# Optimization experiments

Measured on AMD Instinct MI355X. Metric: run time of the kernel, lower is better.

## Reference

```python
import jax, jax.numpy as jnp
import numpy as np

B_SZ, L_MAX, T_LEN, D = 512, 48, 128, 300   # sentences, graph slots, tokens, glove_dim
N_A, N_C = 2048, 2048                        # aspect rows, clause rows
H, TOP_K = 4, 96                             # attention heads, top-k over flattened LxL


def setup_inputs() -> dict:
    key = jax.random.key(0)
    ks = jax.random.split(key, 8)
    input_embed = jax.random.normal(ks[0], (B_SZ, T_LEN, D), jnp.float32)
    clause_output = jax.random.normal(ks[1], (N_C, D), jnp.float32)
    batch_aa_mask = (jax.random.uniform(ks[2], (N_A, T_LEN)) < 0.5).astype(jnp.float32)
    aa_graph_length = jax.random.randint(ks[3], (B_SZ,), 1, L_MAX + 1, dtype=jnp.int32)
    # collision-free scatter destinations; maxima hit B_SZ-1 and L_MAX-1 exactly
    map_AA = jnp.arange(N_A, dtype=jnp.int32) % B_SZ
    map_AA_idx = (4 + jnp.arange(N_A, dtype=jnp.int32) // B_SZ).at[-1].set(L_MAX - 1)
    map_AS = jnp.arange(N_C, dtype=jnp.int32) % B_SZ
    map_AS_idx = jnp.arange(N_C, dtype=jnp.int32) // B_SZ
    sc = 1.0 / np.sqrt(D).astype(np.float32)
    Wq = jax.random.normal(ks[4], (D, D), jnp.float32) * sc
    Wk = jax.random.normal(ks[5], (D, D), jnp.float32) * sc
    Wg = jax.random.normal(ks[6], (D, D), jnp.float32) * sc
    bq = jnp.zeros((D,), jnp.float32)
    bk = jnp.zeros((D,), jnp.float32)
    bg = jnp.zeros((D,), jnp.float32)
    return {"input_embed": input_embed, "clause_output": clause_output,
            "batch_aa_mask": batch_aa_mask, "aa_graph_length": aa_graph_length,
            "map_AA": map_AA, "map_AA_idx": map_AA_idx,
            "map_AS": map_AS, "map_AS_idx": map_AS_idx,
            "Wq": Wq, "bq": bq, "Wk": Wk, "bk": bk, "Wg": Wg, "bg": bg}


def reference(input_embed, clause_output, batch_aa_mask, aa_graph_length,
              map_AA, map_AA_idx, map_AS, map_AS_idx, Wq, bq, Wk, bk, Wg, bg):
    B, L = B_SZ, L_MAX
    dk = D // H
    # gather sentence tokens per aspect, masked sum over tokens -> [Na, D]
    aa_embed = jnp.einsum('ntd,nt->nd', input_embed[map_AA], batch_aa_mask)
    # scatter aspect and clause features into the [B, L, D] graph tensor
    inner = jnp.zeros((B, L, D), input_embed.dtype)
    inner = inner.at[map_AA, map_AA_idx].set(aa_embed)
    inner = inner.at[map_AS, map_AS_idx].set(clause_output)
    mask_indi = (jnp.arange(L)[None, :] < aa_graph_length[:, None]).astype(inner.dtype)  # [B,L]
    # attention-based adjacency (scores only, softmax over keys)
    q = (inner @ Wq.T + bq).reshape(B, L, H, dk).transpose(0, 2, 1, 3)
    k = (inner @ Wk.T + bk).reshape(B, L, H, dk).transpose(0, 2, 1, 3)
    scores = jnp.einsum('bhid,bhjd->bhij', q, k) / jnp.sqrt(jnp.asarray(dk, inner.dtype))
    scores = jnp.where(mask_indi[:, None, None, :] == 0, -1e9, scores)
    attn = jax.nn.softmax(scores, axis=-1)                      # [B,H,L,L]
    # average heads, replace diagonal with self-loops, zero padded rows
    adj = attn.mean(axis=1)
    eye = jnp.eye(L, dtype=adj.dtype)
    adj = adj * (1.0 - eye) + eye
    adj = adj * mask_indi[:, :, None]
    # top-k sparsify over flattened adjacency, symmetrize, diag=1, reweight
    flat = adj.reshape(B, L * L)
    kth = jax.lax.top_k(flat, TOP_K)[0][:, -1]                  # [B]
    sel = (flat >= kth[:, None]).astype(adj.dtype).reshape(B, L, L)
    sel = sel + sel.transpose(0, 2, 1)
    sel = sel * (1.0 - eye) + eye
    adj = sel * adj
    # one GCN layer: relu(W(A x) / (rowsum(A)+1))
    denom = adj.sum(axis=-1, keepdims=True) + 1.0
    gcn = jax.nn.relu((jnp.einsum('bij,bjd->bid', adj, inner) @ Wg.T + bg) / denom)
    # gather back to clause rows; keep clause_output where graph has <=1 node
    aa_out = gcn[map_AS, map_AS_idx]                            # [Nc, D]
    need = (aa_graph_length[map_AS] > 1)[:, None]
    return jnp.where(need, aa_out, clause_output)
```

## Files before the change

### kernel.cpp

```cpp
#include <hip/hip_runtime.h>
#include <math.h>

#define B_SZ 512
#define LG 48
#define T_LEN 128
#define DIM 300
#define NA 2048
#define NC 2048
#define NH 4
#define DK 75
#define KTOP 96
#define ACAP 16
#define TM 64
#define TN 64
#define WSS 156
#define QKS 608
#define GTM 32
#define GTN 64
#define GKC 60
#define FCAP2 9
#define SSTR 612

__global__ __launch_bounds__(256) void build_kernel(
    const int* __restrict__ mapAA, const int* __restrict__ mapAAi,
    int* __restrict__ slot_src, int* __restrict__ acnt, int* __restrict__ alist) {
  int n = blockIdx.x * 256 + threadIdx.x;
  if (n >= NA) return;
  int b = mapAA[n];
  atomicMax(&slot_src[b * LG + mapAAi[n]], n);
  int pos = atomicAdd(&acnt[b], 1);
  if (pos < ACAP) alist[b * ACAP + pos] = n;
}

__global__ __launch_bounds__(256) void aspect_kernel(
    const float* __restrict__ embed, const float* __restrict__ mask,
    const int* __restrict__ acnt, const int* __restrict__ alist,
    float* __restrict__ X) {
  int b = blockIdx.x;
  int na = acnt[b]; if (na > ACAP) na = ACAP;
  if (na == 0) return;
  __shared__ float mLds[ACAP][T_LEN];
  __shared__ float4 eLds[32][DK];
  int tid = threadIdx.x;
  for (int i = tid; i < na * T_LEN; i += 256) {
    int k = i / T_LEN, t = i - k * T_LEN;
    mLds[k][t] = mask[(size_t)alist[b * ACAP + k] * T_LEN + t];
  }
  int nw = na * DK;
  int i0 = tid, i1 = tid + 256;
  int k0 = i0 / DK, d0 = i0 - k0 * DK;
  int k1 = i1 / DK, d1 = i1 - k1 * DK;
  float4 a0 = {0, 0, 0, 0}, a1 = {0, 0, 0, 0};
  const float4* e4 = (const float4*)(embed + (size_t)b * T_LEN * DIM);
  for (int t0 = 0; t0 < T_LEN; t0 += 32) {
    __syncthreads();
    for (int i = tid; i < 32 * DK; i += 256) {
      int t = i / DK, d = i - t * DK;
      eLds[t][d] = e4[(size_t)(t0 + t) * DK + d];
    }
    __syncthreads();
#pragma unroll
    for (int t = 0; t < 32; ++t) {
      if (i0 < nw) {
        float m = mLds[k0][t0 + t]; float4 ev = eLds[t][d0];
        a0.x += m * ev.x; a0.y += m * ev.y; a0.z += m * ev.z; a0.w += m * ev.w;
      }
      if (i1 < nw) {
        float m = mLds[k1][t0 + t]; float4 ev = eLds[t][d1];
        a1.x += m * ev.x; a1.y += m * ev.y; a1.z += m * ev.z; a1.w += m * ev.w;
      }
    }
  }
  if (i0 < nw) ((float4*)(X + (size_t)alist[b * ACAP + k0] * DIM))[d0] = a0;
  if (i1 < nw) ((float4*)(X + (size_t)alist[b * ACAP + k1] * DIM))[d1] = a1;
}

__global__ __launch_bounds__(128) void clause_kernel(
    const float* __restrict__ clause, const int* __restrict__ mapAS,
    const int* __restrict__ mapASi, float* __restrict__ X,
    int* __restrict__ slot_src) {
  int n = blockIdx.x, t = threadIdx.x;
  const float4* src = (const float4*)(clause + (size_t)n * DIM);
  float4* dst = (float4*)(X + (size_t)(NA + n) * DIM);
  if (t < DIM / 4) dst[t] = src[t];
  if (t == 96) atomicMax(&slot_src[mapAS[n] * LG + mapASi[n]], NA + n);
}

__global__ __launch_bounds__(256) void qk_kernel(
    const float* __restrict__ X, const float* __restrict__ Wq,
    const float* __restrict__ Wk, float* __restrict__ QKP) {
  __shared__ __align__(16) float ws[TN][WSS];
  int z = blockIdx.z;
  int kbase = z ? 152 : 0;
  int ng = z ? 37 : 38;
  int m0 = blockIdx.x * TM, n0 = blockIdx.y * TN;
  int tid = threadIdx.x;
  int ty = tid >> 4;
  int tx = tid & 15;
  float acc[4][4];
#pragma unroll
  for (int a = 0; a < 4; ++a)
#pragma unroll
    for (int c = 0; c < 4; ++c) acc[a][c] = 0.f;

  for (int i = tid; i < TN * ng; i += 256) {
    int c = i / ng, g = i - c * ng;
    int col = n0 + c;
    float4 v = {0.f, 0.f, 0.f, 0.f};
    if (col < 2 * DIM) {
      const float* w = (col < DIM) ? (Wq + (size_t)col * DIM)
                                   : (Wk + (size_t)(col - DIM) * DIM);
      v = *(const float4*)&w[kbase + g * 4];
    }
    *(float4*)&ws[c][g * 4] = v;
  }
  __syncthreads();

  const float* xrow[4];
#pragma unroll
  for (int a = 0; a < 4; ++a)
    xrow[a] = X + (size_t)(m0 + ty * 4 + a) * DIM + kbase;

#pragma unroll 2
  for (int kg = 0; kg < ng; ++kg) {
    float4 xv[4], wv[4];
#pragma unroll
    for (int a = 0; a < 4; ++a) xv[a] = *(const float4*)&xrow[a][kg * 4];
#pragma unroll
    for (int c = 0; c < 4; ++c) wv[c] = *(const float4*)&ws[tx + 16 * c][kg * 4];
#pragma unroll
    for (int a = 0; a < 4; ++a)
#pragma unroll
      for (int c = 0; c < 4; ++c)
        acc[a][c] += wv[c].x * xv[a].x + wv[c].y * xv[a].y +
                     wv[c].z * xv[a].z + wv[c].w * xv[a].w;
  }

  float* out = QKP + (size_t)z * (NA + NC) * QKS;
#pragma unroll
  for (int cc = 0; cc < 4; ++cc) {
    int col = n0 + tx + 16 * cc;
    if (col < 2 * DIM) {
      int off;
      if (col < DIM) off = col + col / DK;
      else { int c2 = col - DIM; off = 304 + c2 + c2 / DK; }
#pragma unroll
      for (int a = 0; a < 4; ++a)
        out[(size_t)(m0 + ty * 4 + a) * QKS + off] = acc[a][cc];
    }
  }
}

__global__ __launch_bounds__(512) void attn2_kernel(
    const float* __restrict__ QKP, const float* __restrict__ X,
    const float* __restrict__ bq, const float* __restrict__ bk,
    const int* __restrict__ slot_src, const int* __restrict__ aa_len,
    float* __restrict__ xout, float* __restrict__ dng, int* __restrict__ mdg) {
  int b = blockIdx.x, tid = threadIdx.x;
  __shared__ __align__(16) float staged[FCAP2][SSTR];
  __shared__ float buf4[NH][LG][LG + 1];
  __shared__ float coef[4][LG], denomc[4];
  __shared__ int srcs[LG], nlist[LG], flist[LG], qrow[LG];
  __shared__ float kthL;
  __shared__ int sh_nneed, sh_nf;

  int length = aa_len[b];
  if (length > LG) length = LG;
  if (tid < LG) srcs[tid] = slot_src[b * LG + tid];
  __syncthreads();

  if (tid < 64) {
    bool isneed = (tid < LG) && (srcs[tid] >= NA);
    unsigned long long nm = __ballot(isneed);
    if (isneed) nlist[__popcll(nm & ((1ull << tid) - 1ull))] = tid;
    bool isf = (tid < LG) && (srcs[tid] >= 0);
    unsigned long long fm = __ballot(isf);
    int nf = __popcll(fm);
    if (nf > FCAP2 - 1) nf = FCAP2 - 1;
    if (isf) {
      int c = __popcll(fm & ((1ull << tid) - 1ull));
      if (c < FCAP2 - 1) flist[c] = tid;
    }
    if (tid < LG) {
      int c = __popcll(fm & ((1ull << tid) - 1ull));
      qrow[tid] = (isf && c < FCAP2 - 1) ? c : nf;
    }
    if (tid == 0) { sh_nneed = __popcll(nm); sh_nf = nf; }
  }
  __syncthreads();
  int nneed = sh_nneed, nf = sh_nf;

  if (length <= 1) {
    if (tid < nneed) mdg[srcs[nlist[tid]] - NA] = 0;
    return;
  }

  for (int j = tid; j < 608; j += 512) {
    int half = (j >= 304) ? 1 : 0;
    int jj = j - half * 304;
    int h = jj / 76, d = jj - h * 76;
    float v = 0.f;
    if (d < DK) v = half ? bk[h * DK + d] : bq[h * DK + d];
    staged[nf][j] = v;
  }
  __syncthreads();
  {
    const float* P0 = QKP;
    const float* P1 = QKP + (size_t)(NA + NC) * QKS;
    for (int i = tid; i < nf * 152; i += 512) {
      int m = i / 152, g = i - m * 152;
      size_t base = (size_t)srcs[flist[m]] * QKS + g * 4;
      float4 a = *(const float4*)&P0[base];
      float4 c = *(const float4*)&P1[base];
      float4 bv = *(const float4*)&staged[nf][g * 4];
      float4 v;
      v.x = (a.x + c.x) + bv.x;
      v.y = (a.y + c.y) + bv.y;
      v.z = (a.z + c.z) + bv.z;
      v.w = (a.w + c.w) + bv.w;
      *(float4*)&staged[m][g * 4] = v;
    }
  }
  __syncthreads();
  if (tid < nf * 8) {
    int m = tid >> 3, p = tid & 7;
    int pos = (p & 3) * 76 + 75 + ((p >> 2) * 304);
    staged[m][pos] = 0.f;
  }
  __syncthreads();

  const float sdk = sqrtf((float)DK);
  int h = tid >> 7;
  int t = tid & 127;
  int ti = t >> 3, tj = t & 7;
  int i0 = ti * 3, j0 = tj * 6;

  int qr[3], kr[6];
#pragma unroll
  for (int a = 0; a < 3; ++a) qr[a] = qrow[i0 + a];
#pragma unroll
  for (int c = 0; c < 6; ++c) kr[c] = qrow[j0 + c];

  if (i0 < length) {
    float acc[3][6];
#pragma unroll
    for (int a = 0; a < 3; ++a)
#pragma unroll
      for (int c = 0; c < 6; ++c) acc[a][c] = 0.f;
    for (int d4 = 0; d4 < 19; ++d4) {
      float4 qv[3], kv[6];
#pragma unroll
      for (int a = 0; a < 3; ++a)
        qv[a] = *(const float4*)&staged[qr[a]][h * 76 + d4 * 4];
#pragma unroll
      for (int c = 0; c < 6; ++c)
        kv[c] = *(const float4*)&staged[kr[c]][304 + h * 76 + d4 * 4];
#pragma unroll
      for (int a = 0; a < 3; ++a)
#pragma unroll
        for (int c = 0; c < 6; ++c)
          acc[a][c] += qv[a].x * kv[c].x + qv[a].y * kv[c].y +
                       qv[a].z * kv[c].z + qv[a].w * kv[c].w;
    }
#pragma unroll
    for (int a = 0; a < 3; ++a) {
      float p[6];
#pragma unroll
      for (int c = 0; c < 6; ++c)
        p[c] = (j0 + c < length) ? (acc[a][c] / sdk) : -1e9f;
      float mx = p[0];
#pragma unroll
      for (int c = 1; c < 6; ++c) mx = fmaxf(mx, p[c]);
      mx = fmaxf(mx, __shfl_xor(mx, 1));
      mx = fmaxf(mx, __shfl_xor(mx, 2));
      mx = fmaxf(mx, __shfl_xor(mx, 4));
      float rs = 0.f;
#pragma unroll
      for (int c = 0; c < 6; ++c) { p[c] = expf(p[c] - mx); rs += p[c]; }
      rs += __shfl_xor(rs, 1);
      rs += __shfl_xor(rs, 2);
      rs += __shfl_xor(rs, 4);
      if (i0 + a < length) {
#pragma unroll
        for (int c = 0; c < 6; ++c)
          buf4[h][i0 + a][j0 + c] = p[c] / rs;
      }
    }
  }
  __syncthreads();

  for (int e = tid; e < LG * LG; e += 512) {
    int i = e / LG, j = e - (e / LG) * LG;
    float v = 0.f;
    if (i < length)
      v = ((buf4[0][i][j] + buf4[1][i][j]) +
           (buf4[2][i][j] + buf4[3][i][j])) * 0.25f;
    if (i == j) v = (i < length) ? 1.0f : 0.0f;
    buf4[0][i][j] = v;
  }
  __syncthreads();

  if (tid < 64) {
    unsigned int vb[36];
#pragma unroll
    for (int v = 0; v < 36; ++v) {
      int e = v * 64 + tid;
      vb[v] = __float_as_uint(buf4[0][e / LG][e % LG]);
    }
    unsigned int cur = 0u;
    for (int bit = 30; bit >= 0; --bit) {
      unsigned int cand = cur | (1u << bit);
      int c = 0;
#pragma unroll
      for (int v = 0; v < 36; ++v) c += (vb[v] >= cand) ? 1 : 0;
      c += __shfl_xor(c, 32); c += __shfl_xor(c, 16);
      c += __shfl_xor(c, 8);  c += __shfl_xor(c, 4);
      c += __shfl_xor(c, 2);  c += __shfl_xor(c, 1);
      if (c >= KTOP) cur = cand;
    }
    if (tid == 0) kthL = __uint_as_float(cur);
  }
  __syncthreads();
  const float kth = kthL;

  int nc = (nneed > 4) ? 4 : nneed;
  if (tid < nc * LG) {
    int r = tid / LG, j = tid - (tid / LG) * LG;
    int i = nlist[r];
    float aij = buf4[0][i][j];
    float v;
    if (j == i) v = aij;
    else {
      float selv = (aij >= kth ? 1.f : 0.f) + (buf4[0][j][i] >= kth ? 1.f : 0.f);
      v = selv * aij;
    }
    coef[r][j] = v;
  }
  __syncthreads();
  if (tid < nc) {
    float sm = 0.f;
    for (int j = 0; j < LG; ++j) sm += coef[tid][j];
    denomc[tid] = sm + 1.f;
  }
  __syncthreads();
  for (int w = tid; w < nc * (DIM / 4); w += 512) {
    int r = w / (DIM / 4), d4 = w - (w / (DIM / 4)) * (DIM / 4);
    float4 acc = {0.f, 0.f, 0.f, 0.f};
    for (int m = 0; m < nf; ++m) {
      int j = flist[m];
      float a = coef[r][j];
      float4 xv = ((const float4*)(X + (size_t)srcs[j] * DIM))[d4];
      acc.x += a * xv.x; acc.y += a * xv.y;
      acc.z += a * xv.z; acc.w += a * xv.w;
    }
    int n = srcs[nlist[r]] - NA;
    ((float4*)(xout + (size_t)n * DIM))[d4] = acc;
  }
  if (tid < nc) {
    int n = srcs[nlist[tid]] - NA;
    mdg[n] = 1;
    dng[n] = denomc[tid];
  }
}

__global__ __launch_bounds__(256) void gcn_kernel(
    const float* __restrict__ xg, const float* __restrict__ dng,
    const int* __restrict__ mdg, const float* __restrict__ Wg,
    const float* __restrict__ bg, const float* __restrict__ clause,
    float* __restrict__ out) {
  __shared__ __align__(16) float xs[GTM][GKC];
  __shared__ __align__(16) float ws[GTN][GKC];
  int m0 = blockIdx.x * GTM, n0 = blockIdx.y * GTN;
  int tid = threadIdx.x;
  int ty = tid >> 4;
  int tx = tid & 15;
  float acc[2][4];
#pragma unroll
  for (int a = 0; a < 2; ++a)
#pragma unroll
    for (int c = 0; c < 4; ++c) acc[a][c] = 0.f;

  for (int kc = 0; kc < DIM; kc += GKC) {
    __syncthreads();
    for (int i = tid; i < GTM * (GKC / 4); i += 256) {
      int r = i / (GKC / 4), g = i - r * (GKC / 4);
      *(float4*)&xs[r][g * 4] =
          *(const float4*)&xg[(size_t)(m0 + r) * DIM + kc + g * 4];
    }
    for (int i = tid; i < GTN * (GKC / 4); i += 256) {
      int c = i / (GKC / 4), g = i - c * (GKC / 4);
      int col = n0 + c;
      float4 v = {0.f, 0.f, 0.f, 0.f};
      if (col < DIM)
        v = *(const float4*)&Wg[(size_t)col * DIM + kc + g * 4];
      *(float4*)&ws[c][g * 4] = v;
    }
    __syncthreads();
#pragma unroll 5
    for (int kg = 0; kg < GKC / 4; ++kg) {
      float4 xv[2], wv[4];
#pragma unroll
      for (int a = 0; a < 2; ++a) xv[a] = *(const float4*)&xs[ty * 2 + a][kg * 4];
#pragma unroll
      for (int c = 0; c < 4; ++c) wv[c] = *(const float4*)&ws[tx + 16 * c][kg * 4];
#pragma unroll
      for (int a = 0; a < 2; ++a)
#pragma unroll
        for (int c = 0; c < 4; ++c)
          acc[a][c] += wv[c].x * xv[a].x + wv[c].y * xv[a].y +
                       wv[c].z * xv[a].z + wv[c].w * xv[a].w;
    }
  }

  int md[2]; float dn[2];
#pragma unroll
  for (int a = 0; a < 2; ++a) {
    int row = m0 + ty * 2 + a;
    md[a] = mdg[row];
    dn[a] = dng[row];
  }
#pragma unroll
  for (int cc = 0; cc < 4; ++cc) {
    int col = n0 + tx + 16 * cc;
    if (col < DIM) {
      float bgc = bg[col];
#pragma unroll
      for (int a = 0; a < 2; ++a) {
        int row = m0 + ty * 2 + a;
        float v;
        if (md[a]) v = fmaxf((acc[a][cc] + bgc) / dn[a], 0.f);
        else v = clause[(size_t)row * DIM + col];
        out[(size_t)row * DIM + col] = v;
      }
    }
  }
}

extern "C" void kernel_launch(void* const* d_in, const int* in_sizes, int n_in,
                              void* d_out, int out_size, void* d_ws, size_t ws_size,
                              hipStream_t stream) {
  (void)in_sizes; (void)n_in; (void)out_size; (void)ws_size;
  const float* input_embed = (const float*)d_in[0];
  const float* clause      = (const float*)d_in[1];
  const float* aa_mask     = (const float*)d_in[2];
  const int*   aa_len      = (const int*)d_in[3];
  const int*   map_AA      = (const int*)d_in[4];
  const int*   map_AA_idx  = (const int*)d_in[5];
  const int*   map_AS      = (const int*)d_in[6];
  const int*   map_AS_idx  = (const int*)d_in[7];
  const float* Wq = (const float*)d_in[8];
  const float* bq = (const float*)d_in[9];
  const float* Wk = (const float*)d_in[10];
  const float* bk = (const float*)d_in[11];
  const float* Wg = (const float*)d_in[12];
  const float* bg = (const float*)d_in[13];
  float* out = (float*)d_out;

  float* X   = (float*)d_ws;
  float* QKP = X + (size_t)(NA + NC) * DIM;
  int* slot_src = (int*)(QKP + (size_t)2 * (NA + NC) * QKS);
  int* acnt = slot_src + B_SZ * LG;
  int* alist = acnt + B_SZ;
  float* dng = (float*)alist;
  int* mdg = (int*)(dng + NC);
  float* xg = (float*)(alist + B_SZ * ACAP);

  hipMemsetAsync(slot_src, 0xFF, (size_t)B_SZ * LG * sizeof(int), stream);
  hipMemsetAsync(acnt, 0x00, (size_t)B_SZ * sizeof(int), stream);
  build_kernel<<<(NA + 255) / 256, 256, 0, stream>>>(map_AA, map_AA_idx,
                                                     slot_src, acnt, alist);
  clause_kernel<<<NC, 128, 0, stream>>>(clause, map_AS, map_AS_idx, X, slot_src);
  aspect_kernel<<<B_SZ, 256, 0, stream>>>(input_embed, aa_mask, acnt, alist, X);
  dim3 qkgrid((NA + NC) / TM, (2 * DIM + TN - 1) / TN, 2);
  qk_kernel<<<qkgrid, 256, 0, stream>>>(X, Wq, Wk, QKP);
  attn2_kernel<<<B_SZ, 512, 0, stream>>>(QKP, X, bq, bk, slot_src, aa_len,
                                         xg, dng, mdg);
  dim3 ggrid(NC / GTM, (DIM + GTN - 1) / GTN);
  gcn_kernel<<<ggrid, 256, 0, stream>>>(xg, dng, mdg, Wg, bg, clause, out);
}
```

Baseline: 148.6 us.

## Compute attention rows once per distinct query type in attn2 kernel

Most graph rows in a sentence have identical query vectors, since empty slots all use the bias-only row. The attention kernel now computes softmax rows only for the distinct query types (filled slots plus one empty type) and expands them into the full adjacency through a qrow lookup. The block size drops from 512 to 256 threads and shared memory shrinks, which is meant to cut redundant dot products and softmax work and may allow more resident blocks. The cost is an extra indirection when forming the head-averaged adjacency.

```diff
diff --git a/kernel.cpp b/kernel.cpp
--- a/kernel.cpp
+++ b/kernel.cpp
@@ -20,6 +20,7 @@
 #define GKC 60
 #define FCAP2 9
 #define SSTR 612
+#define NTMAX 10
 
 __global__ __launch_bounds__(256) void build_kernel(
     const int* __restrict__ mapAA, const int* __restrict__ mapAAi,
@@ -151,14 +152,15 @@
   }
 }
 
-__global__ __launch_bounds__(512) void attn2_kernel(
+__global__ __launch_bounds__(256) void attn2_kernel(
     const float* __restrict__ QKP, const float* __restrict__ X,
     const float* __restrict__ bq, const float* __restrict__ bk,
     const int* __restrict__ slot_src, const int* __restrict__ aa_len,
     float* __restrict__ xout, float* __restrict__ dng, int* __restrict__ mdg) {
   int b = blockIdx.x, tid = threadIdx.x;
   __shared__ __align__(16) float staged[FCAP2][SSTR];
-  __shared__ float buf4[NH][LG][LG + 1];
+  __shared__ float st[NH][NTMAX][LG + 1];
+  __shared__ float adj[LG][LG + 1];
   __shared__ float coef[4][LG], denomc[4];
   __shared__ int srcs[LG], nlist[LG], flist[LG], qrow[LG];
   __shared__ float kthL;
@@ -195,7 +197,7 @@
     return;
   }
 
-  for (int j = tid; j < 608; j += 512) {
+  for (int j = tid; j < 608; j += 256) {
     int half = (j >= 304) ? 1 : 0;
     int jj = j - half * 304;
     int h = jj / 76, d = jj - h * 76;
@@ -207,7 +209,7 @@
   {
     const float* P0 = QKP;
     const float* P1 = QKP + (size_t)(NA + NC) * QKS;
-    for (int i = tid; i < nf * 152; i += 512) {
+    for (int i = tid; i < nf * 152; i += 256) {
       int m = i / 152, g = i - m * 152;
       size_t base = (size_t)srcs[flist[m]] * QKS + g * 4;
       float4 a = *(const float4*)&P0[base];
@@ -230,73 +232,66 @@
   __syncthreads();
 
   const float sdk = sqrtf((float)DK);
-  int h = tid >> 7;
-  int t = tid & 127;
-  int ti = t >> 3, tj = t & 7;
-  int i0 = ti * 3, j0 = tj * 6;
-
-  int qr[3], kr[6];
-#pragma unroll
-  for (int a = 0; a < 3; ++a) qr[a] = qrow[i0 + a];
-#pragma unroll
-  for (int c = 0; c < 6; ++c) kr[c] = qrow[j0 + c];
-
-  if (i0 < length) {
-    float acc[3][6];
-#pragma unroll
-    for (int a = 0; a < 3; ++a)
-#pragma unroll
-      for (int c = 0; c < 6; ++c) acc[a][c] = 0.f;
-    for (int d4 = 0; d4 < 19; ++d4) {
-      float4 qv[3], kv[6];
-#pragma unroll
-      for (int a = 0; a < 3; ++a)
-        qv[a] = *(const float4*)&staged[qr[a]][h * 76 + d4 * 4];
-#pragma unroll
-      for (int c = 0; c < 6; ++c)
-        kv[c] = *(const float4*)&staged[kr[c]][304 + h * 76 + d4 * 4];
-#pragma unroll
-      for (int a = 0; a < 3; ++a)
+  int ntypes = nf + 1;
+  {
+    int grp = tid >> 7;
+    int t = tid & 127;
+    int tt = t >> 3;
+    int tj = t & 7;
+    int j0 = tj * 6;
+    int kr[6];
+#pragma unroll
+    for (int c = 0; c < 6; ++c) kr[c] = qrow[j0 + c];
+    for (int it = 0; it < 2; ++it) {
+      int h = grp * 2 + it;
+      if (tt < ntypes) {
+        float acc[6];
+#pragma unroll
+        for (int c = 0; c < 6; ++c) acc[c] = 0.f;
+        for (int d4 = 0; d4 < 19; ++d4) {
+          float4 qv = *(const float4*)&staged[tt][h * 76 + d4 * 4];
+          float4 kv[6];
+#pragma unroll
+          for (int c = 0; c < 6; ++c)
+            kv[c] = *(const float4*)&staged[kr[c]][304 + h * 76 + d4 * 4];
+#pragma unroll
+          for (int c = 0; c < 6; ++c)
+            acc[c] += qv.x * kv[c].x + qv.y * kv[c].y +
+                      qv.z * kv[c].z + qv.w * kv[c].w;
+        }
+        float p[6];
 #pragma unroll
         for (int c = 0; c < 6; ++c)
-          acc[a][c] += qv[a].x * kv[c].x + qv[a].y * kv[c].y +
-                       qv[a].z * kv[c].z + qv[a].w * kv[c].w;
-    }
-#pragma unroll
-    for (int a = 0; a < 3; ++a) {
-      float p[6];
-#pragma unroll
-      for (int c = 0; c < 6; ++c)
-        p[c] = (j0 + c < length) ? (acc[a][c] / sdk) : -1e9f;
-      float mx = p[0];
-#pragma unroll
-      for (int c = 1; c < 6; ++c) mx = fmaxf(mx, p[c]);
-      mx = fmaxf(mx, __shfl_xor(mx, 1));
-      mx = fmaxf(mx, __shfl_xor(mx, 2));
-      mx = fmaxf(mx, __shfl_xor(mx, 4));
-      float rs = 0.f;
-#pragma unroll
-      for (int c = 0; c < 6; ++c) { p[c] = expf(p[c] - mx); rs += p[c]; }
-      rs += __shfl_xor(rs, 1);
-      rs += __shfl_xor(rs, 2);
-      rs += __shfl_xor(rs, 4);
-      if (i0 + a < length) {
-#pragma unroll
-        for (int c = 0; c < 6; ++c)
-          buf4[h][i0 + a][j0 + c] = p[c] / rs;
+          p[c] = (j0 + c < length) ? (acc[c] / sdk) : -1e9f;
+        float mx = p[0];
+#pragma unroll
+        for (int c = 1; c < 6; ++c) mx = fmaxf(mx, p[c]);
+        mx = fmaxf(mx, __shfl_xor(mx, 1));
+        mx = fmaxf(mx, __shfl_xor(mx, 2));
+        mx = fmaxf(mx, __shfl_xor(mx, 4));
+        float rs = 0.f;
+#pragma unroll
+        for (int c = 0; c < 6; ++c) { p[c] = expf(p[c] - mx); rs += p[c]; }
+        rs += __shfl_xor(rs, 1);
+        rs += __shfl_xor(rs, 2);
+        rs += __shfl_xor(rs, 4);
+#pragma unroll
+        for (int c = 0; c < 6; ++c) st[h][tt][j0 + c] = p[c] / rs;
       }
     }
   }
   __syncthreads();
 
-  for (int e = tid; e < LG * LG; e += 512) {
+  for (int e = tid; e < LG * LG; e += 256) {
     int i = e / LG, j = e - (e / LG) * LG;
     float v = 0.f;
-    if (i < length)
-      v = ((buf4[0][i][j] + buf4[1][i][j]) +
-           (buf4[2][i][j] + buf4[3][i][j])) * 0.25f;
+    if (i < length) {
+      int ty = qrow[i];
+      v = ((st[0][ty][j] + st[1][ty][j]) +
+           (st[2][ty][j] + st[3][ty][j])) * 0.25f;
+    }
     if (i == j) v = (i < length) ? 1.0f : 0.0f;
-    buf4[0][i][j] = v;
+    adj[i][j] = v;
   }
   __syncthreads();
 
@@ -305,7 +300,7 @@
 #pragma unroll
     for (int v = 0; v < 36; ++v) {
       int e = v * 64 + tid;
-      vb[v] = __float_as_uint(buf4[0][e / LG][e % LG]);
+      vb[v] = __float_as_uint(adj[e / LG][e % LG]);
     }
     unsigned int cur = 0u;
     for (int bit = 30; bit >= 0; --bit) {
@@ -327,11 +322,11 @@
   if (tid < nc * LG) {
     int r = tid / LG, j = tid - (tid / LG) * LG;
     int i = nlist[r];
-    float aij = buf4[0][i][j];
+    float aij = adj[i][j];
     float v;
     if (j == i) v = aij;
     else {
-      float selv = (aij >= kth ? 1.f : 0.f) + (buf4[0][j][i] >= kth ? 1.f : 0.f);
+      float selv = (aij >= kth ? 1.f : 0.f) + (adj[j][i] >= kth ? 1.f : 0.f);
       v = selv * aij;
     }
     coef[r][j] = v;
@@ -343,7 +338,7 @@
     denomc[tid] = sm + 1.f;
   }
   __syncthreads();
-  for (int w = tid; w < nc * (DIM / 4); w += 512) {
+  for (int w = tid; w < nc * (DIM / 4); w += 256) {
     int r = w / (DIM / 4), d4 = w - (w / (DIM / 4)) * (DIM / 4);
     float4 acc = {0.f, 0.f, 0.f, 0.f};
     for (int m = 0; m < nf; ++m) {
@@ -473,7 +468,7 @@
   aspect_kernel<<<B_SZ, 256, 0, stream>>>(input_embed, aa_mask, acnt, alist, X);
   dim3 qkgrid((NA + NC) / TM, (2 * DIM + TN - 1) / TN, 2);
   qk_kernel<<<qkgrid, 256, 0, stream>>>(X, Wq, Wk, QKP);
-  attn2_kernel<<<B_SZ, 512, 0, stream>>>(QKP, X, bq, bk, slot_src, aa_len,
+  attn2_kernel<<<B_SZ, 256, 0, stream>>>(QKP, X, bq, bk, slot_src, aa_len,
                                          xg, dng, mdg);
   dim3 ggrid(NC / GTM, (DIM + GTN - 1) / GTN);
   gcn_kernel<<<ggrid, 256, 0, stream>>>(xg, dng, mdg, Wg, bg, clause, out);
```

New measurement: 167.5 us. 12.7% more time.
